# Performance work log

Measured on AMD Instinct MI355X. Metric: run time of the kernel, lower is better.

## Reference

```python
import jax, jax.numpy as jnp
import numpy as np
from jax import lax

R = 10          # 10 iterations of (3x3x3 conv > 0) == one binary box dilation of radius 10
TOP_N = 250
SMOOTH = 1e-5
WEIGHT_CE = 1.0
WEIGHT_DICE = 1.0
FR_WEIGHT = 5.0


def _box_dilate(mask, r=R):
    # binary dilation with a (2r+1)^3 box, done separably along D,H,W
    x = mask.astype(jnp.float32)
    for axis in (1, 2, 3):
        win = [1, 1, 1, 1]
        win[axis] = 2 * r + 1
        x = lax.reduce_window(x, 0.0, lax.max, tuple(win), (1, 1, 1, 1), 'SAME')
    return x > 0


def _masked_mean(x, mask):
    cnt = jnp.sum(mask)
    s = jnp.sum(jnp.where(mask, x, 0.0))
    return jnp.where(cnt > 0, s / jnp.maximum(cnt, 1), 0.0)


def _fr_loss(feature, label):
    pos = label[:, 0] == 1                                  # (B,D,H,W)
    neg = label[:, 0] == 0
    f = jnp.moveaxis(feature, 1, -1)                        # (B,D,H,W,C)
    cnt = jnp.sum(pos)
    # mean positive feature (zeros if no positives)
    mean_pos = jnp.sum(jnp.where(pos[..., None], f, 0.0), axis=(0, 1, 2, 3)) / jnp.maximum(cnt, 1)
    std_feat = jnp.where(cnt > 0, mean_pos, 0.0)
    std_n = std_feat / jnp.maximum(jnp.linalg.norm(std_feat), 1e-12)
    # normalized feature map; cosine of a normalized feature with std_n == dot product
    f_n = f / jnp.maximum(jnp.linalg.norm(f, axis=-1, keepdims=True), 1e-12)
    cos_map = jnp.einsum('bdhwc,c->bdhw', f_n, std_n)
    # 1) positive compactness loss
    positive_loss = _masked_mean(1.0 - cos_map, pos)
    easy = _box_dilate(pos) & (~pos)
    mis_loss = _masked_mean(jax.nn.relu(cos_map), easy)
    # 3) hardest negatives: top-250 negative similarities, scatter to mask, dilate
    neg_sims = jnp.where(neg, cos_map, -1e30).reshape(-1)
    top_v, top_i = lax.top_k(neg_sims, TOP_N)
    hi = jnp.zeros(neg_sims.shape, jnp.float32).at[top_i].set((top_v > -1e29).astype(jnp.float32))
    hi = hi.reshape(pos.shape) > 0
    final_neg = _box_dilate(hi) & (~pos)
    neg_loss = _masked_mean(jax.nn.relu(cos_map), final_neg)
    return positive_loss + mis_loss + neg_loss


def _ce_and_dice(net_output, target):
    C = net_output.shape[1]
    logp = jax.nn.log_softmax(net_output, axis=1)           # (B,C,D,H,W)
    ce = -jnp.mean(jnp.take_along_axis(logp, target, axis=1))
    p = jnp.exp(logp)
    y = jax.nn.one_hot(target[:, 0], C, dtype=p.dtype)      # (B,D,H,W,C)
    y = jnp.moveaxis(y, -1, 1)                               # (B,C,D,H,W)
    axes = (0, 2, 3, 4)                                      # batch_dice=True
    tp = jnp.sum(p * y, axes)
    fp = jnp.sum(p * (1.0 - y), axes)
    fn = jnp.sum((1.0 - p) * y, axes)
    dc = (2.0 * tp + SMOOTH) / jnp.maximum(2.0 * tp + fp + fn + SMOOTH, 1e-8)
    dc_loss = -jnp.mean(dc[1:])                              # do_bg=False
    return ce, dc_loss


def setup_inputs() -> dict:
    key = jax.random.key(0)
    k1, k2, k3 = jax.random.split(key, 3)
    B, Cf, Cls, S = 2, 16, 3, 128
    feature = jax.random.normal(k1, (B, Cf, S, S, S), dtype=jnp.float32)
    net_output = jax.random.normal(k2, (B, Cls, S, S, S), dtype=jnp.float32)
    target = jax.random.randint(k3, (B, 1, S, S, S), 0, 3, dtype=jnp.int32)
    return {"feature": feature, "net_output": net_output, "target": target}


def reference(feature, net_output, target):
    ce, dc = _ce_and_dice(net_output, target)
    fr = _fr_loss(feature, target)
    return WEIGHT_CE * ce + WEIGHT_DICE * dc + FR_WEIGHT * fr
```

## Files before the change

### kernel.cpp

```cpp
#include <hip/hip_runtime.h>
#include <hip/hip_bf16.h>
#include <math.h>

#define S3    128
#define NB    2
#define CF    16
#define CHS   (S3*S3*S3)
#define NVOX  (NB*CHS)
#define NW    (NVOX/64)
#define CAP   1048576

typedef unsigned long long u64;
typedef unsigned int u32;
typedef float f4 __attribute__((ext_vector_type(4)));
typedef int   i4 __attribute__((ext_vector_type(4)));

#define ACC_OFF    0
#define STD_OFF    512
#define SCAN_OFF   576
#define HIST_OFF   1024
#define HIB_OFF    (HIST_OFF + 4096*4)
#define ZERO_BYTES (HIB_OFF + NW*8)
#define POSB_OFF   544768
#define NEGB_OFF   (POSB_OFF + NW*8)
#define DTMP_OFF   (NEGB_OFF + NW*8)
#define CAND_OFF   (DTMP_OFF + 2*NW*8)
#define COS_OFF    (CAND_OFF + CAP*8)


__device__ __forceinline__ double wave_red(double x) {
    for (int o = 32; o > 0; o >>= 1) x += __shfl_down(x, o);
    return x;
}
__device__ __forceinline__ u32 mono_key(float f) {
    u32 u = __float_as_uint(f);
    return (u & 0x80000000u) ? ~u : (u | 0x80000000u);
}
__device__ __forceinline__ u64 spread4(u32 x16) {
    u64 x = (u64)(x16 & 0xFFFFu);
    x = (x | (x << 24)) & 0x000000FF000000FFull;
    x = (x | (x << 12)) & 0x000F000F000F000Full;
    x = (x | (x << 6))  & 0x0303030303030303ull;
    x = (x | (x << 3))  & 0x1111111111111111ull;
    return x;
}

template<int NBINS>
__device__ __forceinline__ void sel_desc(const u32* h, u32 need, u32* ss, u32* res)
{
    const int t = threadIdx.x;
    const int CH = NBINS / 256;
    u32 s = 0;
    #pragma unroll
    for (int j = 0; j < CH; j++) s += h[t * CH + j];
    ss[t] = s;
    __syncthreads();
    for (int o = 1; o < 256; o <<= 1) {
        u32 v = (t + o < 256) ? ss[t + o] : 0;
        __syncthreads();
        ss[t] += v;
        __syncthreads();
    }
    u32 above = ss[t] - s;
    if (above < need && above + s >= need) {
        u32 cum = above;
        int bin = t * CH;
        for (int b = t * CH + CH - 1; b >= t * CH; b--) {
            if (cum + h[b] >= need) { bin = b; break; }
            cum += h[b];
        }
        res[0] = (u32)bin;
        res[1] = need - cum;
    }
    __syncthreads();
}

__global__ __launch_bounds__(256) void k_ce(const float* __restrict__ net,
        const int* __restrict__ tgt, u64* __restrict__ posb, u64* __restrict__ negb,
        double* __restrict__ acc)
{
    int tid = blockIdx.x * 256 + threadIdx.x;
    const int gstride = gridDim.x * 256;
    const int lane = threadIdx.x & 63;
    float ce = 0.f, s0 = 0.f, s1 = 0.f, s2 = 0.f, ta0 = 0.f, ta1 = 0.f, ta2 = 0.f;
    int n0 = 0, n1 = 0, n2 = 0;

    for (int idx = tid; idx < NVOX / 4; idx += gstride) {
        const int v4 = idx << 2;
        const int b = v4 >> 21;
        const i4 tv = __builtin_nontemporal_load((const i4*)(tgt + v4));
        const int T[4] = {tv[0], tv[1], tv[2], tv[3]};
        u32 nib_p = (u32)(T[0]==1) | ((u32)(T[1]==1)<<1) | ((u32)(T[2]==1)<<2) | ((u32)(T[3]==1)<<3);
        u32 nib_n = (u32)(T[0]==0) | ((u32)(T[1]==0)<<1) | ((u32)(T[2]==0)<<2) | ((u32)(T[3]==0)<<3);
        int pp = __popc(nib_p), nn_ = __popc(nib_n);
        n1 += pp; n0 += nn_; n2 += 4 - pp - nn_;

        u64 bp0 = __ballot(nib_p & 1), bp1 = __ballot(nib_p & 2),
            bp2 = __ballot(nib_p & 4), bp3 = __ballot(nib_p & 8);
        u64 bn0 = __ballot(nib_n & 1), bn1 = __ballot(nib_n & 2),
            bn2 = __ballot(nib_n & 4), bn3 = __ballot(nib_n & 8);
        if ((lane & 15) == 0) {
            int wsel = lane >> 4, sh = wsel << 4;
            u64 wp = spread4((u32)(bp0 >> sh)) | (spread4((u32)(bp1 >> sh)) << 1)
                   | (spread4((u32)(bp2 >> sh)) << 2) | (spread4((u32)(bp3 >> sh)) << 3);
            u64 wn = spread4((u32)(bn0 >> sh)) | (spread4((u32)(bn1 >> sh)) << 1)
                   | (spread4((u32)(bn2 >> sh)) << 2) | (spread4((u32)(bn3 >> sh)) << 3);
            int wi = ((idx - lane) >> 4) + wsel;
            posb[wi] = wp; negb[wi] = wn;
        }

        const size_t nbase = (size_t)v4 + (size_t)b * (2u * CHS);
        f4 a0 = __builtin_nontemporal_load((const f4*)(net + nbase));
        f4 a1 = __builtin_nontemporal_load((const f4*)(net + nbase + CHS));
        f4 a2 = __builtin_nontemporal_load((const f4*)(net + nbase + 2 * (size_t)CHS));
        #pragma unroll
        for (int j = 0; j < 4; j++) {
            float x0 = a0[j], x1 = a1[j], x2 = a2[j];
            float m = fmaxf(x0, fmaxf(x1, x2));
            float e0 = expf(x0 - m), e1 = expf(x1 - m), e2 = expf(x2 - m);
            float sum = e0 + e1 + e2;
            float lse = m + logf(sum);
            int t = T[j];
            float xt = (t == 0) ? x0 : ((t == 1) ? x1 : x2);
            ce += lse - xt;
            float inv = 1.f / sum;
            float p0 = e0 * inv, p1 = e1 * inv, p2 = e2 * inv;
            s0 += p0; s1 += p1; s2 += p2;
            if (t == 0) ta0 += p0; else if (t == 1) ta1 += p1; else ta2 += p2;
        }
    }

    __shared__ double red[4][10];
    double vals[10] = {(double)n0, (double)n1, (double)n2, (double)ce,
                       (double)s0, (double)s1, (double)s2,
                       (double)ta0, (double)ta1, (double)ta2};
    int wid = threadIdx.x >> 6;
    #pragma unroll
    for (int i = 0; i < 10; i++) {
        double x = wave_red(vals[i]);
        if (lane == 0) red[wid][i] = x;
    }
    __syncthreads();
    if (threadIdx.x < 10) {
        double s = red[0][threadIdx.x] + red[1][threadIdx.x] + red[2][threadIdx.x] + red[3][threadIdx.x];
        atomicAdd(&acc[16 + threadIdx.x], s);
    }
}

__global__ __launch_bounds__(256) void k_pos(const float* __restrict__ feat,
        const u64* __restrict__ posb, double* __restrict__ acc)
{
    int tid = blockIdx.x * 256 + threadIdx.x;
    const int gstride = gridDim.x * 256;
    const int lane = threadIdx.x & 63;
    float fs[16];
    #pragma unroll
    for (int c = 0; c < 16; c++) fs[c] = 0.f;

    for (int idx = tid; idx < NVOX / 4; idx += gstride) {
        const int v4 = idx << 2;
        const int b = v4 >> 21;
        u32 nib = (u32)(posb[v4 >> 6] >> (v4 & 63)) & 0xFu;
        float w0 = (float)(nib & 1), w1 = (float)((nib >> 1) & 1),
              w2 = (float)((nib >> 2) & 1), w3 = (float)((nib >> 3) & 1);
        const float* fb = feat + (size_t)v4 + (size_t)b * ((size_t)(CF - 1) * CHS);
        #pragma unroll
        for (int c = 0; c < 16; c++) {
            f4 f = *(const f4*)(fb + (size_t)c * CHS);
            fs[c] += f[0] * w0 + f[1] * w1 + f[2] * w2 + f[3] * w3;
        }
    }

    __shared__ double red[4][16];
    int wid = threadIdx.x >> 6;
    #pragma unroll
    for (int i = 0; i < 16; i++) {
        double x = wave_red((double)fs[i]);
        if (lane == 0) red[wid][i] = x;
    }
    __syncthreads();
    if (threadIdx.x < 16) {
        double s = red[0][threadIdx.x] + red[1][threadIdx.x] + red[2][threadIdx.x] + red[3][threadIdx.x];
        atomicAdd(&acc[threadIdx.x], s);
    }
}

__global__ void k_std(const double* __restrict__ acc, float* __restrict__ stdn) {
    __shared__ float v[16];
    double cnt = acc[17];
    if (threadIdx.x < 16) {
        double mp = acc[threadIdx.x] / fmax(cnt, 1.0);
        v[threadIdx.x] = (cnt > 0.0) ? (float)mp : 0.0f;
    }
    __syncthreads();
    if (threadIdx.x == 0) {
        float n = 0;
        for (int c = 0; c < 16; c++) n += v[c] * v[c];
        n = fmaxf(sqrtf(n), 1e-12f);
        for (int c = 0; c < 16; c++) stdn[c] = v[c] / n;
    }
}

__global__ __launch_bounds__(256) void k_cos(const float* __restrict__ feat,
        const float* __restrict__ stdn, const u64* __restrict__ negb,
        float* __restrict__ cosm, u32* __restrict__ hist)
{
    __shared__ u32 h[4096];
    __shared__ float sn[16];
    for (int i = threadIdx.x; i < 4096; i += 256) h[i] = 0;
    if (threadIdx.x < 16) sn[threadIdx.x] = stdn[threadIdx.x];
    __syncthreads();
    int tid = blockIdx.x * 256 + threadIdx.x;
    const int gstride = gridDim.x * 256;
    for (int idx = tid; idx < NVOX / 4; idx += gstride) {
        const int v4 = idx << 2;
        const int b = v4 >> 21;
        const float* fb = feat + (size_t)v4 + (size_t)b * ((size_t)(CF - 1) * CHS);
        float d0 = 0, d1 = 0, d2 = 0, d3 = 0, q0 = 0, q1 = 0, q2 = 0, q3 = 0;
        #pragma unroll
        for (int c = 0; c < 16; c++) {
            f4 f = *(const f4*)(fb + (size_t)c * CHS);
            float s = sn[c];
            d0 = fmaf(f[0], s, d0); q0 = fmaf(f[0], f[0], q0);
            d1 = fmaf(f[1], s, d1); q1 = fmaf(f[1], f[1], q1);
            d2 = fmaf(f[2], s, d2); q2 = fmaf(f[2], f[2], q2);
            d3 = fmaf(f[3], s, d3); q3 = fmaf(f[3], f[3], q3);
        }
        f4 cv;
        cv[0] = d0 / fmaxf(sqrtf(q0), 1e-12f);
        cv[1] = d1 / fmaxf(sqrtf(q1), 1e-12f);
        cv[2] = d2 / fmaxf(sqrtf(q2), 1e-12f);
        cv[3] = d3 / fmaxf(sqrtf(q3), 1e-12f);
        __builtin_nontemporal_store(cv, (f4*)(cosm + v4));
        u32 nib = (u32)(negb[v4 >> 6] >> (v4 & 63)) & 0xFu;
        if (nib & 1) atomicAdd(&h[mono_key(cv[0]) >> 20], 1u);
        if (nib & 2) atomicAdd(&h[mono_key(cv[1]) >> 20], 1u);
        if (nib & 4) atomicAdd(&h[mono_key(cv[2]) >> 20], 1u);
        if (nib & 8) atomicAdd(&h[mono_key(cv[3]) >> 20], 1u);
    }
    __syncthreads();
    for (int i = threadIdx.x; i < 4096; i += 256)
        if (h[i]) atomicAdd(&hist[i], h[i]);
}

__global__ __launch_bounds__(256) void k_scanA(const u32* __restrict__ hist, u32* __restrict__ scan) {
    __shared__ u32 h[4096];
    __shared__ u32 ss[256];
    __shared__ u32 res[2];
    for (int i = threadIdx.x; i < 4096; i += 256) h[i] = hist[i];
    __syncthreads();
    sel_desc<4096>(h, 250u, ss, res);
    if (threadIdx.x == 0) { scan[0] = res[0]; scan[1] = res[1]; }
}

__global__ __launch_bounds__(256) void k_collect(const float* __restrict__ cosm,
        const u64* __restrict__ negb, u32* __restrict__ scan, u64* __restrict__ cand)
{
    const u32 thr = scan[0] << 20;
    int tid = blockIdx.x * 256 + threadIdx.x;
    const int gstride = gridDim.x * 256;
    for (int idx = tid; idx < NVOX / 4; idx += gstride) {
        const int v4 = idx << 2;
        u32 nib = (u32)(negb[v4 >> 6] >> (v4 & 63)) & 0xFu;
        if (!nib) continue;
        float4 cv = *(const float4*)(cosm + v4);
        const float C[4] = {cv.x, cv.y, cv.z, cv.w};
        #pragma unroll
        for (int j = 0; j < 4; j++) {
            if ((nib >> j) & 1) {
                u32 key = mono_key(C[j]);
                if (key >= thr) {
                    u32 p = atomicAdd(&scan[4], 1u);
                    if (p < CAP) cand[p] = ((u64)key << 32) | (u32)(v4 + j);
                }
            }
        }
    }
}

__global__ __launch_bounds__(256) void k_select(const u64* __restrict__ cand,
        const u32* __restrict__ scan, u64* __restrict__ hib)
{
    __shared__ u32 h[4096];
    __shared__ u32 ss[256];
    __shared__ u32 res[2];
    __shared__ u32 eqlist[2048];
    __shared__ u32 eqc;
    const u32 cnt = scan[4];
    const int n = (int)(cnt < CAP ? cnt : CAP);
    const u32 binA = scan[0];
    const u32 need1 = scan[1];

    for (int i = threadIdx.x; i < 4096; i += 256) h[i] = 0;
    if (threadIdx.x == 0) eqc = 0;
    __syncthreads();
    for (int i = threadIdx.x; i < n; i += 256) {
        u32 key = (u32)(cand[i] >> 32);
        if ((key >> 20) == binA) atomicAdd(&h[(key >> 8) & 0xFFFu], 1u);
    }
    __syncthreads();
    sel_desc<4096>(h, need1, ss, res);
    const u32 b1 = res[0], need2 = res[1];

    for (int i = threadIdx.x; i < 4096; i += 256) h[i] = 0;
    __syncthreads();
    const u32 pre24 = (binA << 12) | b1;
    for (int i = threadIdx.x; i < n; i += 256) {
        u32 key = (u32)(cand[i] >> 32);
        if ((key >> 8) == pre24) atomicAdd(&h[key & 0xFFu], 1u);
    }
    __syncthreads();
    sel_desc<256>(h, need2, ss, res);
    const u32 K = (pre24 << 8) | res[0];
    const u32 need3 = res[1];

    for (int i = threadIdx.x; i < n; i += 256) {
        u64 code = cand[i];
        u32 key = (u32)(code >> 32), vi = (u32)code;
        if (key > K) atomicOr(&hib[vi >> 6], 1ull << (vi & 63));
        else if (key == K) { u32 p = atomicAdd(&eqc, 1u); if (p < 2048) eqlist[p] = vi; }
    }
    __syncthreads();
    if (threadIdx.x == 0) {
        int m = (int)(eqc < 2048u ? eqc : 2048u);
        u32 prev = 0; bool first = true;
        for (u32 k = 0; k < need3; k++) {
            u32 best = 0xFFFFFFFFu;
            for (int i = 0; i < m; i++) {
                u32 x = eqlist[i];
                if ((first || x > prev) && x < best) best = x;
            }
            if (best == 0xFFFFFFFFu) break;
            atomicOr(&hib[best >> 6], 1ull << (best & 63));
            prev = best; first = false;
        }
    }
}

__global__ __launch_bounds__(256) void k_dilD(const u64* __restrict__ posb,
        const u64* __restrict__ hib, u64* __restrict__ dtmp)
{
    int t = blockIdx.x * 256 + threadIdx.x;
    int m = t >> 16, wI = t & 65535;
    const u64* in = m ? hib : posb;
    int dd = (wI >> 8) & 127;
    int base = wI - (dd << 8);
    int lo = dd > 10 ? dd - 10 : 0, hi2 = dd + 10 > 127 ? 127 : dd + 10;
    u64 r = 0;
    for (int j = lo; j <= hi2; j++) r |= in[base + (j << 8)];
    dtmp[t] = r;
}

__global__ __launch_bounds__(256) void k_dilfin(const u64* __restrict__ dtmp,
        const u64* __restrict__ posb, const float* __restrict__ cosm,
        double* __restrict__ acc)
{
    __shared__ u64 A0[256], A1[256], B0[256], B1[256], E[256], F[256], P[256];
    __shared__ double red[4][5];
    const int s = blockIdx.x;
    const int t = threadIdx.x;
    const int sbase = s * 256;
    A0[t] = dtmp[sbase + t];
    A1[t] = dtmp[65536 + sbase + t];
    P[t]  = posb[sbase + t];
    __syncthreads();
    {
        int hh = t >> 1, col = t & 1;
        int lo = hh > 10 ? hh - 10 : 0, hi2 = hh + 10 > 127 ? 127 : hh + 10;
        u64 r0 = 0, r1 = 0;
        for (int j = lo; j <= hi2; j++) { r0 |= A0[(j << 1) + col]; r1 |= A1[(j << 1) + col]; }
        B0[t] = r0; B1[t] = r1;
    }
    __syncthreads();
    if (t < 128) {
        u64 lo0 = B0[t * 2], hi0 = B0[t * 2 + 1];
        u64 lo1 = B1[t * 2], hi1 = B1[t * 2 + 1];
        u64 rl0 = lo0, rh0 = hi0, rl1 = lo1, rh1 = hi1;
        #pragma unroll
        for (int sft = 1; sft <= 10; sft++) {
            rl0 |= (lo0 << sft) | (lo0 >> sft) | (hi0 << (64 - sft));
            rh0 |= (hi0 << sft) | (hi0 >> sft) | (lo0 >> (64 - sft));
            rl1 |= (lo1 << sft) | (lo1 >> sft) | (hi1 << (64 - sft));
            rh1 |= (hi1 << sft) | (hi1 >> sft) | (lo1 >> (64 - sft));
        }
        E[t * 2] = rl0; E[t * 2 + 1] = rh0;
        F[t * 2] = rl1; F[t * 2 + 1] = rh1;
    }
    __syncthreads();
    float sp = 0.f, se = 0.f, sf = 0.f;
    int cE = 0, cF = 0;
    const float* cbase = cosm + (size_t)s * 16384;
    #pragma unroll 4
    for (int i = 0; i < 16; i++) {
        int q = t + 256 * i;
        int lw = q >> 4, sh = (q & 15) * 4;
        u64 pw = P[lw];
        u32 np_ = (u32)(pw >> sh) & 0xFu;
        u32 ne  = (u32)((E[lw] & ~pw) >> sh) & 0xFu;
        u32 nf  = (u32)((F[lw] & ~pw) >> sh) & 0xFu;
        if (!(np_ | ne | nf)) continue;
        f4 cv = __builtin_nontemporal_load((const f4*)(cbase + q * 4));
        #pragma unroll
        for (int j = 0; j < 4; j++) {
            float cs = cv[j], rl = fmaxf(cs, 0.f);
            if ((np_ >> j) & 1) sp += 1.f - cs;
            if ((ne >> j) & 1) { se += rl; cE++; }
            if ((nf >> j) & 1) { sf += rl; cF++; }
        }
    }
    int lane = t & 63, wid = t >> 6;
    double vals[5] = {(double)sp, (double)se, (double)cE, (double)sf, (double)cF};
    #pragma unroll
    for (int i = 0; i < 5; i++) {
        double x = wave_red(vals[i]);
        if (lane == 0) red[wid][i] = x;
    }
    __syncthreads();
    if (t < 5) {
        double sum = red[0][t] + red[1][t] + red[2][t] + red[3][t];
        atomicAdd(&acc[26 + t], sum);
    }
}

__global__ void k_combine(const double* __restrict__ acc, float* __restrict__ out) {
    if (threadIdx.x != 0 || blockIdx.x != 0) return;
    double ce = acc[19] / (double)NVOX;
    double dcl = 0;
    for (int c = 1; c <= 2; c++) {
        double T = acc[23 + c], S = acc[20 + c], N = acc[16 + c];
        dcl += (2.0 * T + 1e-5) / fmax(S + N + 1e-5, 1e-8);
    }
    double dc_loss = -(dcl / 2.0);
    double cnt = acc[17];
    double pl = (cnt > 0.0) ? acc[26] / fmax(cnt, 1.0) : 0.0;
    double ml = (acc[28] > 0.0) ? acc[27] / acc[28] : 0.0;
    double nl = (acc[30] > 0.0) ? acc[29] / acc[30] : 0.0;
    out[0] = (float)(ce + dc_loss + 5.0 * (pl + ml + nl));
}

extern "C" void kernel_launch(void* const* d_in, const int* in_sizes, int n_in,
                              void* d_out, int out_size, void* d_ws, size_t ws_size,
                              hipStream_t stream)
{
    const float* feat = (const float*)d_in[0];
    const float* net  = (const float*)d_in[1];
    const int*   tgt  = (const int*)d_in[2];
    float* out = (float*)d_out;
    char* w = (char*)d_ws;

    double* acc  = (double*)(w + ACC_OFF);
    float* stdn  = (float*)(w + STD_OFF);
    u32* scan    = (u32*)(w + SCAN_OFF);
    u32* hist    = (u32*)(w + HIST_OFF);
    u64* hib     = (u64*)(w + HIB_OFF);
    u64* posb    = (u64*)(w + POSB_OFF);
    u64* negb    = (u64*)(w + NEGB_OFF);
    u64* dtmp    = (u64*)(w + DTMP_OFF);
    u64* cand    = (u64*)(w + CAND_OFF);
    float* cosm  = (float*)(w + COS_OFF);

    hipMemsetAsync(w, 0, ZERO_BYTES, stream);

    k_ce     <<<2048, 256, 0, stream>>>(net, tgt, posb, negb, acc);
    k_pos    <<<1024, 256, 0, stream>>>(feat, posb, acc);
    k_std    <<<1,    64,  0, stream>>>(acc, stdn);
    k_cos    <<<2048, 256, 0, stream>>>(feat, stdn, negb, cosm, hist);
    k_scanA  <<<1,    256, 0, stream>>>(hist, scan);
    k_collect<<<2048, 256, 0, stream>>>(cosm, negb, scan, cand);
    k_select <<<1,    256, 0, stream>>>(cand, scan, hib);
    k_dilD   <<<512,  256, 0, stream>>>(posb, hib, dtmp);
    k_dilfin <<<256,  256, 0, stream>>>(dtmp, posb, cosm, acc);
    k_combine<<<1,    64,  0, stream>>>(acc, out);
}
```

Before: 207.0 us.

## Split positive-feature sum per channel plane and drop nontemporal cos load

k_pos is restructured so each block handles a single (batch, channel) plane. Each thread accumulates one scalar instead of 16 channel sums, so one block reduction and one atomic replace 16 of each. The grid grows to 4096 blocks for more parallelism and smaller per-thread register state. The mask word is now reloaded once per channel, and the cos-map load in the dilation-finish kernel becomes a regular cached load instead of a nontemporal one.

```diff
diff --git a/kernel.cpp b/kernel.cpp
--- a/kernel.cpp
+++ b/kernel.cpp
@@ -150,39 +150,25 @@
 __global__ __launch_bounds__(256) void k_pos(const float* __restrict__ feat,
         const u64* __restrict__ posb, double* __restrict__ acc)
 {
-    int tid = blockIdx.x * 256 + threadIdx.x;
-    const int gstride = gridDim.x * 256;
-    const int lane = threadIdx.x & 63;
-    float fs[16];
-    #pragma unroll
-    for (int c = 0; c < 16; c++) fs[c] = 0.f;
-
-    for (int idx = tid; idx < NVOX / 4; idx += gstride) {
-        const int v4 = idx << 2;
-        const int b = v4 >> 21;
-        u32 nib = (u32)(posb[v4 >> 6] >> (v4 & 63)) & 0xFu;
-        float w0 = (float)(nib & 1), w1 = (float)((nib >> 1) & 1),
-              w2 = (float)((nib >> 2) & 1), w3 = (float)((nib >> 3) & 1);
-        const float* fb = feat + (size_t)v4 + (size_t)b * ((size_t)(CF - 1) * CHS);
-        #pragma unroll
-        for (int c = 0; c < 16; c++) {
-            f4 f = *(const f4*)(fb + (size_t)c * CHS);
-            fs[c] += f[0] * w0 + f[1] * w1 + f[2] * w2 + f[3] * w3;
-        }
-    }
-
-    __shared__ double red[4][16];
-    int wid = threadIdx.x >> 6;
-    #pragma unroll
-    for (int i = 0; i < 16; i++) {
-        double x = wave_red((double)fs[i]);
-        if (lane == 0) red[wid][i] = x;
-    }
-    __syncthreads();
-    if (threadIdx.x < 16) {
-        double s = red[0][threadIdx.x] + red[1][threadIdx.x] + red[2][threadIdx.x] + red[3][threadIdx.x];
-        atomicAdd(&acc[threadIdx.x], s);
-    }
+    const int plane = blockIdx.x >> 7;
+    const int bp    = blockIdx.x & 127;
+    const int b     = plane >> 4, c = plane & 15;
+    const u64* pb   = posb + (size_t)b * (CHS / 64);
+    const float* fp = feat + (size_t)plane * CHS;
+    float s = 0.f;
+    for (int q = bp * 256 + threadIdx.x; q < CHS / 4; q += 128 * 256) {
+        f4 f = *(const f4*)(fp + (size_t)q * 4);
+        u32 nib = (u32)(pb[q >> 4] >> ((q & 15) * 4)) & 0xFu;
+        s += f[0] * (float)(nib & 1) + f[1] * (float)((nib >> 1) & 1)
+           + f[2] * (float)((nib >> 2) & 1) + f[3] * (float)((nib >> 3) & 1);
+    }
+    __shared__ double red[4];
+    int lane = threadIdx.x & 63, wid = threadIdx.x >> 6;
+    double d = wave_red((double)s);
+    if (lane == 0) red[wid] = d;
+    __syncthreads();
+    if (threadIdx.x == 0)
+        atomicAdd(&acc[c], red[0] + red[1] + red[2] + red[3]);
 }
 
 __global__ void k_std(const double* __restrict__ acc, float* __restrict__ stdn) {
@@ -399,7 +385,7 @@
         u32 ne  = (u32)((E[lw] & ~pw) >> sh) & 0xFu;
         u32 nf  = (u32)((F[lw] & ~pw) >> sh) & 0xFu;
         if (!(np_ | ne | nf)) continue;
-        f4 cv = __builtin_nontemporal_load((const f4*)(cbase + q * 4));
+        f4 cv = *(const f4*)(cbase + q * 4);
         #pragma unroll
         for (int j = 0; j < 4; j++) {
             float cs = cv[j], rl = fmaxf(cs, 0.f);
@@ -462,7 +448,7 @@
     hipMemsetAsync(w, 0, ZERO_BYTES, stream);
 
     k_ce     <<<2048, 256, 0, stream>>>(net, tgt, posb, negb, acc);
-    k_pos    <<<1024, 256, 0, stream>>>(feat, posb, acc);
+    k_pos    <<<4096, 256, 0, stream>>>(feat, posb, acc);
     k_std    <<<1,    64,  0, stream>>>(acc, stdn);
     k_cos    <<<2048, 256, 0, stream>>>(feat, stdn, negb, cosm, hist);
     k_scanA  <<<1,    256, 0, stream>>>(hist, scan);
```

Result: slower. 212.3 us (+2.6%).

## Split CE out of mask kernel, reschedule it last, and flatten k_pos grid

Applied to the files above, without the earlier changes.

Separates the mask/count building from the softmax CE/dice computation. k_mask now reads only the targets, so the feature-side chain (pos sum, cosine, top-k, dilation) can start sooner. The CE kernel moves to the end of the stream. Nontemporal loads and stores on the cosine map and targets are replaced with normal cached accesses, so cosm and tgt can stay in the large last-level cache for the later readers. k_pos drops its grid-stride loop for one vec4 per thread, with each half-block handling 8 channels over 8192 blocks, which adds more atomics and re-reads the targets.

```diff
diff --git a/kernel.cpp b/kernel.cpp
--- a/kernel.cpp
+++ b/kernel.cpp
@@ -75,26 +75,21 @@
     __syncthreads();
 }
 
-__global__ __launch_bounds__(256) void k_ce(const float* __restrict__ net,
-        const int* __restrict__ tgt, u64* __restrict__ posb, u64* __restrict__ negb,
-        double* __restrict__ acc)
+__global__ __launch_bounds__(256) void k_mask(const int* __restrict__ tgt,
+        u64* __restrict__ posb, u64* __restrict__ negb, double* __restrict__ acc)
 {
     int tid = blockIdx.x * 256 + threadIdx.x;
     const int gstride = gridDim.x * 256;
     const int lane = threadIdx.x & 63;
-    float ce = 0.f, s0 = 0.f, s1 = 0.f, s2 = 0.f, ta0 = 0.f, ta1 = 0.f, ta2 = 0.f;
     int n0 = 0, n1 = 0, n2 = 0;
-
     for (int idx = tid; idx < NVOX / 4; idx += gstride) {
         const int v4 = idx << 2;
-        const int b = v4 >> 21;
-        const i4 tv = __builtin_nontemporal_load((const i4*)(tgt + v4));
+        const i4 tv = *(const i4*)(tgt + v4);
         const int T[4] = {tv[0], tv[1], tv[2], tv[3]};
         u32 nib_p = (u32)(T[0]==1) | ((u32)(T[1]==1)<<1) | ((u32)(T[2]==1)<<2) | ((u32)(T[3]==1)<<3);
         u32 nib_n = (u32)(T[0]==0) | ((u32)(T[1]==0)<<1) | ((u32)(T[2]==0)<<2) | ((u32)(T[3]==0)<<3);
         int pp = __popc(nib_p), nn_ = __popc(nib_n);
         n1 += pp; n0 += nn_; n2 += 4 - pp - nn_;
-
         u64 bp0 = __ballot(nib_p & 1), bp1 = __ballot(nib_p & 2),
             bp2 = __ballot(nib_p & 4), bp3 = __ballot(nib_p & 8);
         u64 bn0 = __ballot(nib_n & 1), bn1 = __ballot(nib_n & 2),
@@ -108,81 +103,52 @@
             int wi = ((idx - lane) >> 4) + wsel;
             posb[wi] = wp; negb[wi] = wn;
         }
-
-        const size_t nbase = (size_t)v4 + (size_t)b * (2u * CHS);
-        f4 a0 = __builtin_nontemporal_load((const f4*)(net + nbase));
-        f4 a1 = __builtin_nontemporal_load((const f4*)(net + nbase + CHS));
-        f4 a2 = __builtin_nontemporal_load((const f4*)(net + nbase + 2 * (size_t)CHS));
-        #pragma unroll
-        for (int j = 0; j < 4; j++) {
-            float x0 = a0[j], x1 = a1[j], x2 = a2[j];
-            float m = fmaxf(x0, fmaxf(x1, x2));
-            float e0 = expf(x0 - m), e1 = expf(x1 - m), e2 = expf(x2 - m);
-            float sum = e0 + e1 + e2;
-            float lse = m + logf(sum);
-            int t = T[j];
-            float xt = (t == 0) ? x0 : ((t == 1) ? x1 : x2);
-            ce += lse - xt;
-            float inv = 1.f / sum;
-            float p0 = e0 * inv, p1 = e1 * inv, p2 = e2 * inv;
-            s0 += p0; s1 += p1; s2 += p2;
-            if (t == 0) ta0 += p0; else if (t == 1) ta1 += p1; else ta2 += p2;
-        }
-    }
-
-    __shared__ double red[4][10];
-    double vals[10] = {(double)n0, (double)n1, (double)n2, (double)ce,
-                       (double)s0, (double)s1, (double)s2,
-                       (double)ta0, (double)ta1, (double)ta2};
+    }
+    __shared__ double red[4][3];
+    double vals[3] = {(double)n0, (double)n1, (double)n2};
     int wid = threadIdx.x >> 6;
     #pragma unroll
-    for (int i = 0; i < 10; i++) {
+    for (int i = 0; i < 3; i++) {
         double x = wave_red(vals[i]);
         if (lane == 0) red[wid][i] = x;
     }
     __syncthreads();
-    if (threadIdx.x < 10) {
+    if (threadIdx.x < 3) {
         double s = red[0][threadIdx.x] + red[1][threadIdx.x] + red[2][threadIdx.x] + red[3][threadIdx.x];
         atomicAdd(&acc[16 + threadIdx.x], s);
     }
 }
 
-__global__ __launch_bounds__(256) void k_pos(const float* __restrict__ feat,
+__global__ __launch_bounds__(256, 8) void k_pos(const float* __restrict__ feat,
         const u64* __restrict__ posb, double* __restrict__ acc)
 {
-    int tid = blockIdx.x * 256 + threadIdx.x;
-    const int gstride = gridDim.x * 256;
-    const int lane = threadIdx.x & 63;
-    float fs[16];
-    #pragma unroll
-    for (int c = 0; c < 16; c++) fs[c] = 0.f;
-
-    for (int idx = tid; idx < NVOX / 4; idx += gstride) {
-        const int v4 = idx << 2;
-        const int b = v4 >> 21;
-        u32 nib = (u32)(posb[v4 >> 6] >> (v4 & 63)) & 0xFu;
-        float w0 = (float)(nib & 1), w1 = (float)((nib >> 1) & 1),
-              w2 = (float)((nib >> 2) & 1), w3 = (float)((nib >> 3) & 1);
-        const float* fb = feat + (size_t)v4 + (size_t)b * ((size_t)(CF - 1) * CHS);
-        #pragma unroll
-        for (int c = 0; c < 16; c++) {
-            f4 f = *(const f4*)(fb + (size_t)c * CHS);
-            fs[c] += f[0] * w0 + f[1] * w1 + f[2] * w2 + f[3] * w3;
-        }
-    }
-
-    __shared__ double red[4][16];
-    int wid = threadIdx.x >> 6;
-    #pragma unroll
-    for (int i = 0; i < 16; i++) {
+    const int half = threadIdx.x >> 7;
+    const int q = blockIdx.x * 128 + (threadIdx.x & 127);
+    const int v4 = q << 2;
+    const int b = v4 >> 21;
+    u32 nib = (u32)(posb[v4 >> 6] >> (v4 & 63)) & 0xFu;
+    float w0 = (float)(nib & 1), w1 = (float)((nib >> 1) & 1),
+          w2 = (float)((nib >> 2) & 1), w3 = (float)((nib >> 3) & 1);
+    const float* fb = feat + (size_t)v4 + (size_t)b * ((size_t)(CF - 1) * CHS)
+                    + (size_t)(half * 8) * CHS;
+    float fs[8];
+    #pragma unroll
+    for (int c = 0; c < 8; c++) {
+        f4 f = *(const f4*)(fb + (size_t)c * CHS);
+        fs[c] = f[0] * w0 + f[1] * w1 + f[2] * w2 + f[3] * w3;
+    }
+    __shared__ double red[4][8];
+    int lane = threadIdx.x & 63, wid = threadIdx.x >> 6;
+    #pragma unroll
+    for (int i = 0; i < 8; i++) {
         double x = wave_red((double)fs[i]);
         if (lane == 0) red[wid][i] = x;
     }
     __syncthreads();
-    if (threadIdx.x < 16) {
-        double s = red[0][threadIdx.x] + red[1][threadIdx.x] + red[2][threadIdx.x] + red[3][threadIdx.x];
-        atomicAdd(&acc[threadIdx.x], s);
-    }
+    if (threadIdx.x < 8)
+        atomicAdd(&acc[threadIdx.x], red[0][threadIdx.x] + red[1][threadIdx.x]);
+    else if (threadIdx.x < 16)
+        atomicAdd(&acc[threadIdx.x], red[2][threadIdx.x - 8] + red[3][threadIdx.x - 8]);
 }
 
 __global__ void k_std(const double* __restrict__ acc, float* __restrict__ stdn) {
@@ -231,7 +197,7 @@
         cv[1] = d1 / fmaxf(sqrtf(q1), 1e-12f);
         cv[2] = d2 / fmaxf(sqrtf(q2), 1e-12f);
         cv[3] = d3 / fmaxf(sqrtf(q3), 1e-12f);
-        __builtin_nontemporal_store(cv, (f4*)(cosm + v4));
+        *(f4*)(cosm + v4) = cv;
         u32 nib = (u32)(negb[v4 >> 6] >> (v4 & 63)) & 0xFu;
         if (nib & 1) atomicAdd(&h[mono_key(cv[0]) >> 20], 1u);
         if (nib & 2) atomicAdd(&h[mono_key(cv[1]) >> 20], 1u);
@@ -263,12 +229,11 @@
         const int v4 = idx << 2;
         u32 nib = (u32)(negb[v4 >> 6] >> (v4 & 63)) & 0xFu;
         if (!nib) continue;
-        float4 cv = *(const float4*)(cosm + v4);
-        const float C[4] = {cv.x, cv.y, cv.z, cv.w};
+        f4 cv = *(const f4*)(cosm + v4);
         #pragma unroll
         for (int j = 0; j < 4; j++) {
             if ((nib >> j) & 1) {
-                u32 key = mono_key(C[j]);
+                u32 key = mono_key(cv[j]);
                 if (key >= thr) {
                     u32 p = atomicAdd(&scan[4], 1u);
                     if (p < CAP) cand[p] = ((u64)key << 32) | (u32)(v4 + j);
@@ -399,7 +364,7 @@
         u32 ne  = (u32)((E[lw] & ~pw) >> sh) & 0xFu;
         u32 nf  = (u32)((F[lw] & ~pw) >> sh) & 0xFu;
         if (!(np_ | ne | nf)) continue;
-        f4 cv = __builtin_nontemporal_load((const f4*)(cbase + q * 4));
+        f4 cv = *(const f4*)(cbase + q * 4);
         #pragma unroll
         for (int j = 0; j < 4; j++) {
             float cs = cv[j], rl = fmaxf(cs, 0.f);
@@ -419,6 +384,54 @@
     if (t < 5) {
         double sum = red[0][t] + red[1][t] + red[2][t] + red[3][t];
         atomicAdd(&acc[26 + t], sum);
+    }
+}
+
+__global__ __launch_bounds__(256) void k_ce(const float* __restrict__ net,
+        const int* __restrict__ tgt, double* __restrict__ acc)
+{
+    int tid = blockIdx.x * 256 + threadIdx.x;
+    const int gstride = gridDim.x * 256;
+    const int lane = threadIdx.x & 63;
+    float ce = 0.f, s0 = 0.f, s1 = 0.f, s2 = 0.f, ta0 = 0.f, ta1 = 0.f, ta2 = 0.f;
+    for (int idx = tid; idx < NVOX / 4; idx += gstride) {
+        const int v4 = idx << 2;
+        const int b = v4 >> 21;
+        const i4 tv = *(const i4*)(tgt + v4);
+        const int T[4] = {tv[0], tv[1], tv[2], tv[3]};
+        const size_t nbase = (size_t)v4 + (size_t)b * (2u * CHS);
+        f4 a0 = *(const f4*)(net + nbase);
+        f4 a1 = *(const f4*)(net + nbase + CHS);
+        f4 a2 = *(const f4*)(net + nbase + 2 * (size_t)CHS);
+        #pragma unroll
+        for (int j = 0; j < 4; j++) {
+            float x0 = a0[j], x1 = a1[j], x2 = a2[j];
+            float m = fmaxf(x0, fmaxf(x1, x2));
+            float e0 = expf(x0 - m), e1 = expf(x1 - m), e2 = expf(x2 - m);
+            float sum = e0 + e1 + e2;
+            float lse = m + logf(sum);
+            int t = T[j];
+            float xt = (t == 0) ? x0 : ((t == 1) ? x1 : x2);
+            ce += lse - xt;
+            float inv = 1.f / sum;
+            float p0 = e0 * inv, p1 = e1 * inv, p2 = e2 * inv;
+            s0 += p0; s1 += p1; s2 += p2;
+            if (t == 0) ta0 += p0; else if (t == 1) ta1 += p1; else ta2 += p2;
+        }
+    }
+    __shared__ double red[4][7];
+    double vals[7] = {(double)ce, (double)s0, (double)s1, (double)s2,
+                      (double)ta0, (double)ta1, (double)ta2};
+    int wid = threadIdx.x >> 6;
+    #pragma unroll
+    for (int i = 0; i < 7; i++) {
+        double x = wave_red(vals[i]);
+        if (lane == 0) red[wid][i] = x;
+    }
+    __syncthreads();
+    if (threadIdx.x < 7) {
+        double s = red[0][threadIdx.x] + red[1][threadIdx.x] + red[2][threadIdx.x] + red[3][threadIdx.x];
+        atomicAdd(&acc[19 + threadIdx.x], s);
     }
 }
 
@@ -461,8 +474,8 @@
 
     hipMemsetAsync(w, 0, ZERO_BYTES, stream);
 
-    k_ce     <<<2048, 256, 0, stream>>>(net, tgt, posb, negb, acc);
-    k_pos    <<<1024, 256, 0, stream>>>(feat, posb, acc);
+    k_mask   <<<2048, 256, 0, stream>>>(tgt, posb, negb, acc);
+    k_pos    <<<8192, 256, 0, stream>>>(feat, posb, acc);
     k_std    <<<1,    64,  0, stream>>>(acc, stdn);
     k_cos    <<<2048, 256, 0, stream>>>(feat, stdn, negb, cosm, hist);
     k_scanA  <<<1,    256, 0, stream>>>(hist, scan);
@@ -470,5 +483,6 @@
     k_select <<<1,    256, 0, stream>>>(cand, scan, hib);
     k_dilD   <<<512,  256, 0, stream>>>(posb, hib, dtmp);
     k_dilfin <<<256,  256, 0, stream>>>(dtmp, posb, cosm, acc);
+    k_ce     <<<2048, 256, 0, stream>>>(net, tgt, acc);
     k_combine<<<1,    64,  0, stream>>>(acc, out);
 }
```

New measurement: 293.7 us. 1.42x slower.
